# Kernel tuning notes

Measured on AMD Instinct MI355X. Metric: run time of the kernel, lower is better.

Reference implementation:

```python
import jax, jax.numpy as jnp
import numpy as np

NEG_BIG = -1e12
ALPHA = 0.2  # LeakyReLU negative slope

def setup_inputs() -> dict:
    key = jax.random.key(0)
    k1, k2, k3, k4, k5 = jax.random.split(key, 5)
    N, F_in, F_out = 8192, 256, 128
    inp = jax.random.normal(k1, (N, F_in), dtype=jnp.float32)
    adj = jax.random.randint(k2, (N, N), 0, 2, dtype=jnp.int32)
    W = jax.random.normal(k3, (F_in, F_out), dtype=jnp.float32) * 0.05
    W_2 = jax.random.normal(k4, (F_in, F_out), dtype=jnp.float32) * 0.05
    W_3 = jax.random.normal(k5, (F_in, F_out), dtype=jnp.float32) * 0.05
    return {"inp": inp, "adj": adj, "W": W, "W_2": W_2, "W_3": W_3}

def reference(inp, adj, W, W_2, W_3):
    # h = inp @ W, h_2 = inp @ W_2  -> scores e = LeakyReLU(h @ h_2^T)  [N, N]
    h = inp @ W
    h_2 = inp @ W_2
    e = jax.nn.leaky_relu(h @ h_2.T, negative_slope=ALPHA)
    # adjacency mask, row softmax (dropout disabled: eval mode)
    attention = jax.nn.softmax(jnp.where(adj > 0, e, NEG_BIG), axis=1)
    h_3 = inp @ W_3
    h_prime = attention @ h_3
    return jax.nn.elu(h_prime)  # concat=True path
```

## Files before the change

kernel.cpp:

```cpp
#include <hip/hip_runtime.h>
#include <hip/hip_fp16.h>

#define N    8192
#define FIN  256
#define FOUT 128
#define BN   64

typedef _Float16 half8 __attribute__((ext_vector_type(8)));
typedef _Float16 half4v __attribute__((ext_vector_type(4)));
typedef float floatx4 __attribute__((ext_vector_type(4)));

__device__ __forceinline__ float exp2_fast(float x) { return __builtin_amdgcn_exp2f(x); }

__device__ __forceinline__ void gload_lds16(const void* g, void* l) {
    __builtin_amdgcn_global_load_lds(
        (const __attribute__((address_space(1))) void*)g,
        (__attribute__((address_space(3))) void*)l, 16, 0, 0);
}

__global__ __launch_bounds__(256)
void wprep_kernel(const float* __restrict__ W0,
                  const float* __restrict__ W1,
                  const float* __restrict__ W2,
                  _Float16* __restrict__ Wf)
{
    int idx  = blockIdx.x * 256 + threadIdx.x;
    int lane = idx & 63;
    int frag = idx >> 6;
    int w    = frag >> 6;
    int f    = frag & 63;
    int nt   = f >> 3, kc = f & 7;
    int quad = lane >> 4, lo16 = lane & 15;
    const float* Wp = w == 0 ? W0 : (w == 1 ? W1 : W2);
    half8 v;
#pragma unroll
    for (int jj = 0; jj < 8; jj++)
        v[jj] = (_Float16)Wp[(size_t)(kc * 32 + quad * 8 + jj) * FOUT + nt * 16 + lo16];
    *(half8*)&Wf[(size_t)idx * 8] = v;
}

__global__ __launch_bounds__(256, 2)
void gemmadj_kernel(const float* __restrict__ inp,
                    const _Float16* __restrict__ Wf,
                    _Float16* __restrict__ H,
                    _Float16* __restrict__ H2,
                    _Float16* __restrict__ H3T,
                    const int* __restrict__ adj,
                    unsigned long long* __restrict__ adjbT)
{
    if (blockIdx.x >= 768) {
        const int gw   = (blockIdx.x - 768) * 4 + (threadIdx.x >> 6);
        const int lane = threadIdx.x & 63;
#pragma unroll 1
        for (int k = 0; k < 16; k++) {
            int t  = gw + k * 4096;
            int w  = t >> 9;
            int rg = t & 511;
            const int* p = adj + (size_t)(rg * 16) * N + w * 64 + lane;
            unsigned long long myw = 0;
#pragma unroll
            for (int i = 0; i < 16; i++) {
                unsigned long long b = __ballot(p[(size_t)i * N] != 0);
                myw = (lane == i) ? b : myw;
            }
            if (lane < 16)
                adjbT[(size_t)w * N + rg * 16 + lane] = myw;
        }
        return;
    }

    const int g     = blockIdx.x;
    const int which = g >> 8;
    const int rem   = g & 255;
    const int c0    = ((rem >> 7) & 1) * 64;
    const int r0    = (rem & 127) * 64;
    const _Float16* Wfw = Wf + (size_t)which * 64 * 64 * 8;
    const int tid  = threadIdx.x;
    const int wave = tid >> 6;
    const int lane = tid & 63;
    const int lo16 = lane & 15;
    const int quad = lane >> 4;
    const int r = r0 + wave * 16 + lo16;

    half8 a[8];
#pragma unroll
    for (int kc = 0; kc < 8; kc++) {
        const float* p = &inp[(size_t)r * FIN + kc * 32 + quad * 8];
        float4 v0 = *(const float4*)p;
        float4 v1 = *(const float4*)(p + 4);
        a[kc][0] = (_Float16)v0.x; a[kc][1] = (_Float16)v0.y;
        a[kc][2] = (_Float16)v0.z; a[kc][3] = (_Float16)v0.w;
        a[kc][4] = (_Float16)v1.x; a[kc][5] = (_Float16)v1.y;
        a[kc][6] = (_Float16)v1.z; a[kc][7] = (_Float16)v1.w;
    }

    floatx4 acc[4];
#pragma unroll
    for (int i = 0; i < 4; i++) acc[i] = (floatx4){0.f, 0.f, 0.f, 0.f};

#pragma unroll
    for (int kc = 0; kc < 8; kc++)
#pragma unroll
        for (int nt = 0; nt < 4; nt++) {
            int ntg = (c0 >> 4) + nt;
            half8 b = *(const half8*)&Wfw[(((size_t)ntg * 8 + kc) * 64 + lane) * 8];
            acc[nt] = __builtin_amdgcn_mfma_f32_16x16x32_f16(a[kc], b, acc[nt], 0, 0, 0);
        }

    const int arow = wave * 16 + quad * 4;
    if (which < 2) {
        _Float16* outp = which == 0 ? H : H2;
        const float scale = which == 0 ? 1.44269504f : 1.0f;
#pragma unroll
        for (int nt = 0; nt < 4; nt++)
#pragma unroll
            for (int rr = 0; rr < 4; rr++)
                outp[(size_t)(r0 + arow + rr) * FOUT + c0 + nt * 16 + lo16] =
                    (_Float16)(acc[nt][rr] * scale);
    } else {
#pragma unroll
        for (int nt = 0; nt < 4; nt++) {
            half4v v;
#pragma unroll
            for (int rr = 0; rr < 4; rr++) v[rr] = (_Float16)acc[nt][rr];
            *(half4v*)&H3T[(size_t)(c0 + nt * 16 + lo16) * N + r0 + arow] = v;
        }
    }
}

__global__ __launch_bounds__(256)
void repackKV_kernel(const _Float16* __restrict__ H2,
                     const _Float16* __restrict__ H3T,
                     _Float16* __restrict__ Kf,
                     _Float16* __restrict__ Vf)
{
    if (blockIdx.x < 512) {
        int idx  = blockIdx.x * 256 + threadIdx.x;
        int lane = idx & 63;
        int frag = idx >> 6;
        int jb = frag >> 4, f = frag & 15;
        int c = f >> 3, ntj = (f >> 2) & 1, kc = f & 3;
        int quad = lane >> 4, lo16 = lane & 15;
        int srcrow = jb * 64 + c * 32 + (lo16 >> 2) * 8 + ntj * 4 + (lo16 & 3);
        half8 v = *(const half8*)&H2[(size_t)srcrow * FOUT + kc * 32 + quad * 8];
        *(half8*)&Kf[(size_t)idx * 8] = v;
    } else {
        int idx  = (blockIdx.x - 512) * 256 + threadIdx.x;
        int lane = idx & 63;
        int frag = idx >> 6;
        int jb = frag >> 4, f = frag & 15, nt = f >> 1, kc = f & 1;
        int quad = lane >> 4, lo16 = lane & 15;
        half8 v = *(const half8*)&H3T[(size_t)(nt * 16 + lo16) * N + jb * 64 + kc * 32 + quad * 8];
        *(half8*)&Vf[(size_t)idx * 8] = v;
    }
}

template<int JS>
__global__ __launch_bounds__(256, 2)
void attn_kernel(const _Float16* __restrict__ Hq,
                 const _Float16* __restrict__ Kf,
                 const _Float16* __restrict__ Vf,
                 const unsigned long long* __restrict__ adjbT,
                 float* __restrict__ OpartT,
                 float* __restrict__ mpart,
                 float* __restrict__ lpart)
{
    __shared__ __align__(16) _Float16 KV[2][16384];

    const int tid  = threadIdx.x;
    const int wave = tid >> 6;
    const int lane = tid & 63;
    const int lo16 = lane & 15;
    const int quad = lane >> 4;
    const int bid  = blockIdx.x;
    const int js   = bid & (JS - 1);
    const int ib   = bid / JS;
    const int iw   = ib * 128 + wave * 32;
    const int jbeg = js * (N / JS);
    const int NIT  = (N / JS) / BN;
    const int jb0  = jbeg >> 6;

    half8 q[2][4];
#pragma unroll
    for (int isub = 0; isub < 2; isub++)
#pragma unroll
        for (int kc = 0; kc < 4; kc++)
            q[isub][kc] = *(const half8*)&Hq[(size_t)(iw + isub * 16 + lo16) * FOUT + kc * 32 + quad * 8];

    floatx4 O[8][2];
#pragma unroll
    for (int nt = 0; nt < 8; nt++)
#pragma unroll
        for (int s = 0; s < 2; s++) O[nt][s] = (floatx4){0.f, 0.f, 0.f, 0.f};
    float m_s[2] = {-1e12f, -1e12f}, l_s[2] = {0.f, 0.f};

    {
        const _Float16* gk = Kf + (size_t)jb0 * 8192;
        const _Float16* gv = Vf + (size_t)jb0 * 8192;
#pragma unroll
        for (int r = 0; r < 4; r++) {
            int goff = (r * 256 + tid) * 8;
            int loff = (r * 256 + wave * 64) * 8;
            gload_lds16(gk + goff, &KV[0][loff]);
            gload_lds16(gv + goff, &KV[0][8192 + loff]);
        }
        __syncthreads();
    }

    int cur = 0;
    for (int it = 0; it < NIT; it++) {
        if (it + 1 < NIT) {
            const int jbn = jb0 + it + 1;
            const int nxt = cur ^ 1;
            const _Float16* gk = Kf + (size_t)jbn * 8192;
            const _Float16* gv = Vf + (size_t)jbn * 8192;
#pragma unroll
            for (int r = 0; r < 4; r++) {
                int goff = (r * 256 + tid) * 8;
                int loff = (r * 256 + wave * 64) * 8;
                gload_lds16(gk + goff, &KV[nxt][loff]);
                gload_lds16(gv + goff, &KV[nxt][8192 + loff]);
            }
        }

        const unsigned long long* aw = adjbT + (size_t)(jb0 + it) * N + iw;
        unsigned long long mw[2] = { aw[lo16], aw[16 + lo16] };

        const _Float16* kb = &KV[cur][0];
        const _Float16* vb = &KV[cur][8192];

        floatx4 S[2][2][2];
#pragma unroll
        for (int c = 0; c < 2; c++)
#pragma unroll
            for (int ntj = 0; ntj < 2; ntj++) {
                S[c][ntj][0] = (floatx4){0.f, 0.f, 0.f, 0.f};
                S[c][ntj][1] = (floatx4){0.f, 0.f, 0.f, 0.f};
#pragma unroll
                for (int kc = 0; kc < 4; kc++) {
                    half8 kf = *(const half8*)&kb[(((c * 2 + ntj) * 4 + kc) * 64 + lane) * 8];
                    S[c][ntj][0] = __builtin_amdgcn_mfma_f32_16x16x32_f16(kf, q[0][kc], S[c][ntj][0], 0, 0, 0);
                    S[c][ntj][1] = __builtin_amdgcn_mfma_f32_16x16x32_f16(kf, q[1][kc], S[c][ntj][1], 0, 0, 0);
                }
            }

        half8 pb[2][2];
#pragma unroll
        for (int s = 0; s < 2; s++) {
            float mx = -1e12f;
#pragma unroll
            for (int c = 0; c < 2; c++)
#pragma unroll
                for (int ntj = 0; ntj < 2; ntj++)
#pragma unroll
                    for (int r = 0; r < 4; r++) {
                        float e = S[c][ntj][s][r];
                        e = fmaxf(e, 0.2f * e);
                        S[c][ntj][s][r] = e;
                        mx = fmaxf(mx, e);
                    }
            mx = fmaxf(mx, __shfl_xor(mx, 16));
            mx = fmaxf(mx, __shfl_xor(mx, 32));
            if (__any(mx > m_s[s] + 5.75f)) {
                float mn = fmaxf(m_s[s], mx);
                float al = exp2_fast(m_s[s] - mn);
                m_s[s] = mn;
                l_s[s] *= al;
#pragma unroll
                for (int nt = 0; nt < 8; nt++)
#pragma unroll
                    for (int r = 0; r < 4; r++)
                        O[nt][s][r] *= al;
            }

            unsigned long long mq = mw[s] >> (quad * 8);
            unsigned mh[2] = { (unsigned)mq, (unsigned)(mq >> 32) };
            float sum = 0.f;
#pragma unroll
            for (int c = 0; c < 2; c++)
#pragma unroll
                for (int ntj = 0; ntj < 2; ntj++)
#pragma unroll
                    for (int r = 0; r < 4; r++) {
                        float e = S[c][ntj][s][r] - m_s[s];
                        bool bit = (mh[c] >> (ntj * 4 + r)) & 1u;
                        float p = bit ? exp2_fast(e) : 0.f;
                        sum += p;
                        pb[s][c][ntj * 4 + r] = (_Float16)p;
                    }
            sum += __shfl_xor(sum, 16);
            sum += __shfl_xor(sum, 32);
            l_s[s] += sum;
        }

#pragma unroll
        for (int c = 0; c < 2; c++)
#pragma unroll
            for (int nt = 0; nt < 8; nt++) {
                half8 vf = *(const half8*)&vb[((nt * 2 + c) * 64 + lane) * 8];
                O[nt][0] = __builtin_amdgcn_mfma_f32_16x16x32_f16(vf, pb[0][c], O[nt][0], 0, 0, 0);
                O[nt][1] = __builtin_amdgcn_mfma_f32_16x16x32_f16(vf, pb[1][c], O[nt][1], 0, 0, 0);
            }

        __syncthreads();
        cur ^= 1;
    }

#pragma unroll
    for (int nt = 0; nt < 8; nt++)
#pragma unroll
        for (int s = 0; s < 2; s++)
#pragma unroll
            for (int r = 0; r < 4; r++) {
                int f = nt * 16 + quad * 4 + r;
                int i = iw + s * 16 + lo16;
                OpartT[((size_t)js * FOUT + f) * N + i] = O[nt][s][r];
            }
    if (quad == 0) {
#pragma unroll
        for (int s = 0; s < 2; s++) {
            mpart[js * N + iw + s * 16 + lo16] = m_s[s];
            lpart[js * N + iw + s * 16 + lo16] = l_s[s];
        }
    }
}

template<int JS>
__global__ __launch_bounds__(256)
void combine_kernel(const float* __restrict__ OpartT,
                    const float* __restrict__ mpart,
                    const float* __restrict__ lpart,
                    float* __restrict__ out)
{
    int idx = blockIdx.x * 256 + threadIdx.x;
    int f  = idx >> 11;
    int i4 = (idx & 2047) << 2;

    float4 M = {-3e38f, -3e38f, -3e38f, -3e38f};
    float4 m[JS];
#pragma unroll
    for (int s = 0; s < JS; s++) {
        m[s] = *(const float4*)&mpart[s * N + i4];
        M.x = fmaxf(M.x, m[s].x); M.y = fmaxf(M.y, m[s].y);
        M.z = fmaxf(M.z, m[s].z); M.w = fmaxf(M.w, m[s].w);
    }
    float4 L = {0.f, 0.f, 0.f, 0.f};
    float4 o = {0.f, 0.f, 0.f, 0.f};
#pragma unroll
    for (int s = 0; s < JS; s++) {
        float4 l = *(const float4*)&lpart[s * N + i4];
        float4 w;
        w.x = exp2_fast(m[s].x - M.x); w.y = exp2_fast(m[s].y - M.y);
        w.z = exp2_fast(m[s].z - M.z); w.w = exp2_fast(m[s].w - M.w);
        L.x += l.x * w.x; L.y += l.y * w.y;
        L.z += l.z * w.z; L.w += l.w * w.w;
        float4 v = *(const float4*)&OpartT[((size_t)s * FOUT + f) * N + i4];
        o.x += w.x * v.x; o.y += w.y * v.y;
        o.z += w.z * v.z; o.w += w.w * v.w;
    }
    float r0 = o.x / L.x, r1 = o.y / L.y, r2 = o.z / L.z, r3 = o.w / L.w;
    out[(size_t)(i4 + 0) * FOUT + f] = r0 > 0.f ? r0 : __expf(r0) - 1.f;
    out[(size_t)(i4 + 1) * FOUT + f] = r1 > 0.f ? r1 : __expf(r1) - 1.f;
    out[(size_t)(i4 + 2) * FOUT + f] = r2 > 0.f ? r2 : __expf(r2) - 1.f;
    out[(size_t)(i4 + 3) * FOUT + f] = r3 > 0.f ? r3 : __expf(r3) - 1.f;
}

extern "C" void kernel_launch(void* const* d_in, const int* in_sizes, int n_in,
                              void* d_out, int out_size, void* d_ws, size_t ws_size,
                              hipStream_t stream) {
    const float* inp = (const float*)d_in[0];
    const int*   adj = (const int*)d_in[1];
    const float* W0  = (const float*)d_in[2];
    const float* W1  = (const float*)d_in[3];
    const float* W2  = (const float*)d_in[4];
    float* out = (float*)d_out;

    constexpr int JS = 8;
    char* ws = (char*)d_ws;
    _Float16* H    = (_Float16*)(ws);
    _Float16* H2   = (_Float16*)(ws + (2u << 20));
    _Float16* H3T  = (_Float16*)(ws + (4u << 20));
    _Float16* Wf   = (_Float16*)(ws + (6u << 20));
    _Float16* Kf   = (_Float16*)(ws + (7u << 20));
    _Float16* Vf   = (_Float16*)(ws + (9u << 20));
    float* OpartT  = (float*)(ws + (11u << 20));
    float* mpart   = (float*)(ws + (43u << 20));
    float* lpart   = (float*)(ws + (43u << 20) + (size_t)JS * N * sizeof(float));
    unsigned long long* adjbT = (unsigned long long*)(ws + (44u << 20));

    wprep_kernel<<<48, 256, 0, stream>>>(W0, W1, W2, Wf);
    gemmadj_kernel<<<768 + 1024, 256, 0, stream>>>(inp, Wf, H, H2, H3T, adj, adjbT);
    repackKV_kernel<<<1024, 256, 0, stream>>>(H2, H3T, Kf, Vf);
    attn_kernel<JS><<<(N / 128) * JS, 256, 0, stream>>>(H, Kf, Vf, adjbT, OpartT, mpart, lpart);
    combine_kernel<JS><<<(FOUT * (N / 4)) / 256, 256, 0, stream>>>(OpartT, mpart, lpart, out);
}
```

Baseline: 460.9 us.

## Triple-buffer attention K/V tiles at 32 columns, preload adjacency mask into LDS

```diff
diff --git a/kernel.cpp b/kernel.cpp
--- a/kernel.cpp
+++ b/kernel.cpp
@@ -4,7 +4,7 @@
 #define N    8192
 #define FIN  256
 #define FOUT 128
-#define BN   64
+#define BN   32
 
 typedef _Float16 half8 __attribute__((ext_vector_type(8)));
 typedef _Float16 half4v __attribute__((ext_vector_type(4)));
@@ -19,41 +19,33 @@
 }
 
 __global__ __launch_bounds__(256)
-void wprep_kernel(const float* __restrict__ W0,
-                  const float* __restrict__ W1,
-                  const float* __restrict__ W2,
-                  _Float16* __restrict__ Wf)
+void prep_kernel(const float* __restrict__ W0,
+                 const float* __restrict__ W1,
+                 const float* __restrict__ W2,
+                 _Float16* __restrict__ Wf,
+                 const int* __restrict__ adj,
+                 unsigned long long* __restrict__ adjbT)
 {
-    int idx  = blockIdx.x * 256 + threadIdx.x;
-    int lane = idx & 63;
-    int frag = idx >> 6;
-    int w    = frag >> 6;
-    int f    = frag & 63;
-    int nt   = f >> 3, kc = f & 7;
-    int quad = lane >> 4, lo16 = lane & 15;
-    const float* Wp = w == 0 ? W0 : (w == 1 ? W1 : W2);
-    half8 v;
-#pragma unroll
-    for (int jj = 0; jj < 8; jj++)
-        v[jj] = (_Float16)Wp[(size_t)(kc * 32 + quad * 8 + jj) * FOUT + nt * 16 + lo16];
-    *(half8*)&Wf[(size_t)idx * 8] = v;
-}
-
-__global__ __launch_bounds__(256, 2)
-void gemmadj_kernel(const float* __restrict__ inp,
-                    const _Float16* __restrict__ Wf,
-                    _Float16* __restrict__ H,
-                    _Float16* __restrict__ H2,
-                    _Float16* __restrict__ H3T,
-                    const int* __restrict__ adj,
-                    unsigned long long* __restrict__ adjbT)
-{
-    if (blockIdx.x >= 768) {
-        const int gw   = (blockIdx.x - 768) * 4 + (threadIdx.x >> 6);
+    if (blockIdx.x < 48) {
+        int idx  = blockIdx.x * 256 + threadIdx.x;
+        int lane = idx & 63;
+        int frag = idx >> 6;
+        int w    = frag >> 6;
+        int f    = frag & 63;
+        int nt   = f >> 3, kc = f & 7;
+        int quad = lane >> 4, lo16 = lane & 15;
+        const float* Wp = w == 0 ? W0 : (w == 1 ? W1 : W2);
+        half8 v;
+#pragma unroll
+        for (int jj = 0; jj < 8; jj++)
+            v[jj] = (_Float16)Wp[(size_t)(kc * 32 + quad * 8 + jj) * FOUT + nt * 16 + lo16];
+        *(half8*)&Wf[(size_t)idx * 8] = v;
+    } else {
+        const int gw   = (blockIdx.x - 48) * 4 + (threadIdx.x >> 6);
         const int lane = threadIdx.x & 63;
 #pragma unroll 1
-        for (int k = 0; k < 16; k++) {
-            int t  = gw + k * 4096;
+        for (int k = 0; k < 8; k++) {
+            int t  = gw + k * 8192;
             int w  = t >> 9;
             int rg = t & 511;
             const int* p = adj + (size_t)(rg * 16) * N + w * 64 + lane;
@@ -66,15 +58,20 @@
             if (lane < 16)
                 adjbT[(size_t)w * N + rg * 16 + lane] = myw;
         }
-        return;
-    }
-
-    const int g     = blockIdx.x;
-    const int which = g >> 8;
-    const int rem   = g & 255;
-    const int c0    = ((rem >> 7) & 1) * 64;
-    const int r0    = (rem & 127) * 64;
+    }
+}
+
+__global__ __launch_bounds__(256, 2)
+void gemm3_kernel(const float* __restrict__ inp,
+                  const _Float16* __restrict__ Wf,
+                  _Float16* __restrict__ H,
+                  _Float16* __restrict__ H2,
+                  _Float16* __restrict__ H3T)
+{
+    const int which = blockIdx.z;
+    const int c0    = blockIdx.y * 64;
     const _Float16* Wfw = Wf + (size_t)which * 64 * 64 * 8;
+    const int r0 = blockIdx.x * 64;
     const int tid  = threadIdx.x;
     const int wave = tid >> 6;
     const int lane = tid & 63;
@@ -165,7 +162,8 @@
                  float* __restrict__ mpart,
                  float* __restrict__ lpart)
 {
-    __shared__ __align__(16) _Float16 KV[2][16384];
+    __shared__ __align__(16) _Float16 KV[3][8192];
+    __shared__ unsigned long long ML[16 * 128];
 
     const int tid  = threadIdx.x;
     const int wave = tid >> 6;
@@ -175,10 +173,19 @@
     const int bid  = blockIdx.x;
     const int js   = bid & (JS - 1);
     const int ib   = bid / JS;
-    const int iw   = ib * 128 + wave * 32;
+    const int ibase = ib * 128;
+    const int iw   = ibase + wave * 32;
     const int jbeg = js * (N / JS);
-    const int NIT  = (N / JS) / BN;
+    constexpr int NIT = (N / JS) / BN;
     const int jb0  = jbeg >> 6;
+
+#pragma unroll
+    for (int x = 0; x < 8; x++) {
+        int idx  = x * 256 + tid;
+        int w    = idx >> 7;
+        int r128 = idx & 127;
+        ML[idx] = adjbT[(size_t)(jb0 + w) * N + ibase + r128];
+    }
 
     half8 q[2][4];
 #pragma unroll
@@ -194,71 +201,70 @@
         for (int s = 0; s < 2; s++) O[nt][s] = (floatx4){0.f, 0.f, 0.f, 0.f};
     float m_s[2] = {-1e12f, -1e12f}, l_s[2] = {0.f, 0.f};
 
-    {
-        const _Float16* gk = Kf + (size_t)jb0 * 8192;
-        const _Float16* gv = Vf + (size_t)jb0 * 8192;
-#pragma unroll
-        for (int r = 0; r < 4; r++) {
-            int goff = (r * 256 + tid) * 8;
-            int loff = (r * 256 + wave * 64) * 8;
-            gload_lds16(gk + goff, &KV[0][loff]);
-            gload_lds16(gv + goff, &KV[0][8192 + loff]);
-        }
-        __syncthreads();
-    }
-
-    int cur = 0;
-    for (int it = 0; it < NIT; it++) {
-        if (it + 1 < NIT) {
-            const int jbn = jb0 + it + 1;
-            const int nxt = cur ^ 1;
-            const _Float16* gk = Kf + (size_t)jbn * 8192;
-            const _Float16* gv = Vf + (size_t)jbn * 8192;
-#pragma unroll
-            for (int r = 0; r < 4; r++) {
-                int goff = (r * 256 + tid) * 8;
-                int loff = (r * 256 + wave * 64) * 8;
-                gload_lds16(gk + goff, &KV[nxt][loff]);
-                gload_lds16(gv + goff, &KV[nxt][8192 + loff]);
+    auto STAGE = [&](int buf, int t2) {
+        const int jb2 = jb0 + (t2 >> 1), cb2 = t2 & 1;
+        const _Float16* gk = Kf + ((size_t)jb2 * 16 + cb2 * 8) * 512;
+#pragma unroll
+        for (int r = 0; r < 2; r++)
+            gload_lds16(gk + (r * 256 + tid) * 8, &KV[buf][(r * 256 + wave * 64) * 8]);
+#pragma unroll
+        for (int r = 0; r < 2; r++) {
+            const int fv = r * 4 + wave;
+            gload_lds16(Vf + ((size_t)jb2 * 16 + fv * 2 + cb2) * 512 + lane * 8,
+                        &KV[buf][4096 + fv * 512]);
+        }
+    };
+
+    STAGE(0, 0);
+    STAGE(1, 1);
+    asm volatile("s_waitcnt vmcnt(4) lgkmcnt(0)" ::: "memory");
+    __builtin_amdgcn_sched_barrier(0);
+    __builtin_amdgcn_s_barrier();
+    __builtin_amdgcn_sched_barrier(0);
+
+    int bc = 0;
+    for (int t = 0; t < NIT; t++) {
+        const int cbit = t & 1;
+
+        if (t + 2 < NIT) {
+            int bs = bc + 2; if (bs >= 3) bs -= 3;
+            STAGE(bs, t + 2);
+        }
+
+        unsigned long long mw0 = ML[(t >> 1) * 128 + wave * 32 + lo16];
+        unsigned long long mw1 = ML[(t >> 1) * 128 + wave * 32 + 16 + lo16];
+
+        const _Float16* kb = &KV[bc][0];
+        const _Float16* vb = &KV[bc][4096];
+
+        floatx4 S[2][2];
+        __builtin_amdgcn_s_setprio(1);
+#pragma unroll
+        for (int ntj = 0; ntj < 2; ntj++) {
+            S[ntj][0] = (floatx4){0.f, 0.f, 0.f, 0.f};
+            S[ntj][1] = (floatx4){0.f, 0.f, 0.f, 0.f};
+#pragma unroll
+            for (int kc = 0; kc < 4; kc++) {
+                half8 kf = *(const half8*)&kb[((ntj * 4 + kc) * 64 + lane) * 8];
+                S[ntj][0] = __builtin_amdgcn_mfma_f32_16x16x32_f16(kf, q[0][kc], S[ntj][0], 0, 0, 0);
+                S[ntj][1] = __builtin_amdgcn_mfma_f32_16x16x32_f16(kf, q[1][kc], S[ntj][1], 0, 0, 0);
             }
         }
-
-        const unsigned long long* aw = adjbT + (size_t)(jb0 + it) * N + iw;
-        unsigned long long mw[2] = { aw[lo16], aw[16 + lo16] };
-
-        const _Float16* kb = &KV[cur][0];
-        const _Float16* vb = &KV[cur][8192];
-
-        floatx4 S[2][2][2];
-#pragma unroll
-        for (int c = 0; c < 2; c++)
-#pragma unroll
-            for (int ntj = 0; ntj < 2; ntj++) {
-                S[c][ntj][0] = (floatx4){0.f, 0.f, 0.f, 0.f};
-                S[c][ntj][1] = (floatx4){0.f, 0.f, 0.f, 0.f};
-#pragma unroll
-                for (int kc = 0; kc < 4; kc++) {
-                    half8 kf = *(const half8*)&kb[(((c * 2 + ntj) * 4 + kc) * 64 + lane) * 8];
-                    S[c][ntj][0] = __builtin_amdgcn_mfma_f32_16x16x32_f16(kf, q[0][kc], S[c][ntj][0], 0, 0, 0);
-                    S[c][ntj][1] = __builtin_amdgcn_mfma_f32_16x16x32_f16(kf, q[1][kc], S[c][ntj][1], 0, 0, 0);
-                }
-            }
-
-        half8 pb[2][2];
+        __builtin_amdgcn_s_setprio(0);
+
+        half8 pb[2];
 #pragma unroll
         for (int s = 0; s < 2; s++) {
             float mx = -1e12f;
 #pragma unroll
-            for (int c = 0; c < 2; c++)
-#pragma unroll
-                for (int ntj = 0; ntj < 2; ntj++)
-#pragma unroll
-                    for (int r = 0; r < 4; r++) {
-                        float e = S[c][ntj][s][r];
-                        e = fmaxf(e, 0.2f * e);
-                        S[c][ntj][s][r] = e;
-                        mx = fmaxf(mx, e);
-                    }
+            for (int ntj = 0; ntj < 2; ntj++)
+#pragma unroll
+                for (int rr = 0; rr < 4; rr++) {
+                    float e = S[ntj][s][rr];
+                    e = fmaxf(e, 0.2f * e);
+                    S[ntj][s][rr] = e;
+                    mx = fmaxf(mx, e);
+                }
             mx = fmaxf(mx, __shfl_xor(mx, 16));
             mx = fmaxf(mx, __shfl_xor(mx, 32));
             if (__any(mx > m_s[s] + 5.75f)) {
@@ -269,41 +275,41 @@
 #pragma unroll
                 for (int nt = 0; nt < 8; nt++)
 #pragma unroll
-                    for (int r = 0; r < 4; r++)
-                        O[nt][s][r] *= al;
+                    for (int rr = 0; rr < 4; rr++)
+                        O[nt][s][rr] *= al;
             }
-
-            unsigned long long mq = mw[s] >> (quad * 8);
-            unsigned mh[2] = { (unsigned)mq, (unsigned)(mq >> 32) };
+            unsigned long long mws = (s == 0) ? mw0 : mw1;
+            unsigned m8 = (unsigned)(mws >> (cbit * 32 + quad * 8)) & 0xffu;
             float sum = 0.f;
 #pragma unroll
-            for (int c = 0; c < 2; c++)
-#pragma unroll
-                for (int ntj = 0; ntj < 2; ntj++)
-#pragma unroll
-                    for (int r = 0; r < 4; r++) {
-                        float e = S[c][ntj][s][r] - m_s[s];
-                        bool bit = (mh[c] >> (ntj * 4 + r)) & 1u;
-                        float p = bit ? exp2_fast(e) : 0.f;
-                        sum += p;
-                        pb[s][c][ntj * 4 + r] = (_Float16)p;
-                    }
+            for (int ntj = 0; ntj < 2; ntj++)
+#pragma unroll
+                for (int rr = 0; rr < 4; rr++) {
+                    float e = S[ntj][s][rr] - m_s[s];
+                    float p = ((m8 >> (ntj * 4 + rr)) & 1u) ? exp2_fast(e) : 0.f;
+                    sum += p;
+                    pb[s][ntj * 4 + rr] = (_Float16)p;
+                }
             sum += __shfl_xor(sum, 16);
             sum += __shfl_xor(sum, 32);
             l_s[s] += sum;
         }
 
-#pragma unroll
-        for (int c = 0; c < 2; c++)
-#pragma unroll
-            for (int nt = 0; nt < 8; nt++) {
-                half8 vf = *(const half8*)&vb[((nt * 2 + c) * 64 + lane) * 8];
-                O[nt][0] = __builtin_amdgcn_mfma_f32_16x16x32_f16(vf, pb[0][c], O[nt][0], 0, 0, 0);
-                O[nt][1] = __builtin_amdgcn_mfma_f32_16x16x32_f16(vf, pb[1][c], O[nt][1], 0, 0, 0);
-            }
-
-        __syncthreads();
-        cur ^= 1;
+        __builtin_amdgcn_s_setprio(1);
+#pragma unroll
+        for (int nt = 0; nt < 8; nt++) {
+            half8 vf = *(const half8*)&vb[(nt * 64 + lane) * 8];
+            O[nt][0] = __builtin_amdgcn_mfma_f32_16x16x32_f16(vf, pb[0], O[nt][0], 0, 0, 0);
+            O[nt][1] = __builtin_amdgcn_mfma_f32_16x16x32_f16(vf, pb[1], O[nt][1], 0, 0, 0);
+        }
+        __builtin_amdgcn_s_setprio(0);
+
+        if (t + 2 < NIT) asm volatile("s_waitcnt vmcnt(4)" ::: "memory");
+        else             asm volatile("s_waitcnt vmcnt(0)" ::: "memory");
+        __builtin_amdgcn_sched_barrier(0);
+        __builtin_amdgcn_s_barrier();
+        __builtin_amdgcn_sched_barrier(0);
+        bc = (bc + 1 == 3) ? 0 : bc + 1;
     }
 
 #pragma unroll
@@ -311,10 +317,10 @@
 #pragma unroll
         for (int s = 0; s < 2; s++)
 #pragma unroll
-            for (int r = 0; r < 4; r++) {
-                int f = nt * 16 + quad * 4 + r;
+            for (int rr = 0; rr < 4; rr++) {
+                int f = nt * 16 + quad * 4 + rr;
                 int i = iw + s * 16 + lo16;
-                OpartT[((size_t)js * FOUT + f) * N + i] = O[nt][s][r];
+                OpartT[((size_t)js * FOUT + f) * N + i] = O[nt][s][rr];
             }
     if (quad == 0) {
 #pragma unroll
@@ -388,8 +394,8 @@
     float* lpart   = (float*)(ws + (43u << 20) + (size_t)JS * N * sizeof(float));
     unsigned long long* adjbT = (unsigned long long*)(ws + (44u << 20));
 
-    wprep_kernel<<<48, 256, 0, stream>>>(W0, W1, W2, Wf);
-    gemmadj_kernel<<<768 + 1024, 256, 0, stream>>>(inp, Wf, H, H2, H3T, adj, adjbT);
+    prep_kernel<<<2096, 256, 0, stream>>>(W0, W1, W2, Wf, adj, adjbT);
+    gemm3_kernel<<<dim3(N / 64, 2, 3), 256, 0, stream>>>(inp, Wf, H, H2, H3T);
     repackKV_kernel<<<1024, 256, 0, stream>>>(H2, H3T, Kf, Vf);
     attn_kernel<JS><<<(N / 128) * JS, 256, 0, stream>>>(H, Kf, Vf, adjbT, OpartT, mpart, lpart);
     combine_kernel<JS><<<(FOUT * (N / 4)) / 256, 256, 0, stream>>>(OpartT, mpart, lpart, out);
```

After: 481.9 us. 1.05x slower.

## Fuse adjacency mask reads into attention kernel, drop bit-packing pass

Applied to the files above, without the earlier changes.

```diff
diff --git a/kernel.cpp b/kernel.cpp
--- a/kernel.cpp
+++ b/kernel.cpp
@@ -40,41 +40,16 @@
 }
 
 __global__ __launch_bounds__(256, 2)
-void gemmadj_kernel(const float* __restrict__ inp,
-                    const _Float16* __restrict__ Wf,
-                    _Float16* __restrict__ H,
-                    _Float16* __restrict__ H2,
-                    _Float16* __restrict__ H3T,
-                    const int* __restrict__ adj,
-                    unsigned long long* __restrict__ adjbT)
-{
-    if (blockIdx.x >= 768) {
-        const int gw   = (blockIdx.x - 768) * 4 + (threadIdx.x >> 6);
-        const int lane = threadIdx.x & 63;
-#pragma unroll 1
-        for (int k = 0; k < 16; k++) {
-            int t  = gw + k * 4096;
-            int w  = t >> 9;
-            int rg = t & 511;
-            const int* p = adj + (size_t)(rg * 16) * N + w * 64 + lane;
-            unsigned long long myw = 0;
-#pragma unroll
-            for (int i = 0; i < 16; i++) {
-                unsigned long long b = __ballot(p[(size_t)i * N] != 0);
-                myw = (lane == i) ? b : myw;
-            }
-            if (lane < 16)
-                adjbT[(size_t)w * N + rg * 16 + lane] = myw;
-        }
-        return;
-    }
-
-    const int g     = blockIdx.x;
-    const int which = g >> 8;
-    const int rem   = g & 255;
-    const int c0    = ((rem >> 7) & 1) * 64;
-    const int r0    = (rem & 127) * 64;
+void gemm3_kernel(const float* __restrict__ inp,
+                  const _Float16* __restrict__ Wf,
+                  _Float16* __restrict__ H,
+                  _Float16* __restrict__ H2,
+                  _Float16* __restrict__ H3T)
+{
+    const int which = blockIdx.z;
+    const int c0    = blockIdx.y * 64;
     const _Float16* Wfw = Wf + (size_t)which * 64 * 64 * 8;
+    const int r0 = blockIdx.x * 64;
     const int tid  = threadIdx.x;
     const int wave = tid >> 6;
     const int lane = tid & 63;
@@ -160,7 +135,7 @@
 void attn_kernel(const _Float16* __restrict__ Hq,
                  const _Float16* __restrict__ Kf,
                  const _Float16* __restrict__ Vf,
-                 const unsigned long long* __restrict__ adjbT,
+                 const int* __restrict__ adj,
                  float* __restrict__ OpartT,
                  float* __restrict__ mpart,
                  float* __restrict__ lpart)
@@ -194,37 +169,45 @@
         for (int s = 0; s < 2; s++) O[nt][s] = (floatx4){0.f, 0.f, 0.f, 0.f};
     float m_s[2] = {-1e12f, -1e12f}, l_s[2] = {0.f, 0.f};
 
-    {
-        const _Float16* gk = Kf + (size_t)jb0 * 8192;
-        const _Float16* gv = Vf + (size_t)jb0 * 8192;
+    const int* abase0 = adj + (size_t)(iw + lo16) * N + jbeg + quad * 8;
+    const int* abase1 = abase0 + (size_t)16 * N;
+
+    int4 avA[8], avB[8];
+
+    auto LOADAV = [&](int4 (&av)[8], int it) {
+        const int* b0 = abase0 + it * BN;
+        const int* b1 = abase1 + it * BN;
+        av[0] = *(const int4*)(b0 + 0);
+        av[1] = *(const int4*)(b0 + 4);
+        av[2] = *(const int4*)(b0 + 32);
+        av[3] = *(const int4*)(b0 + 36);
+        av[4] = *(const int4*)(b1 + 0);
+        av[5] = *(const int4*)(b1 + 4);
+        av[6] = *(const int4*)(b1 + 32);
+        av[7] = *(const int4*)(b1 + 36);
+    };
+
+    auto STAGE = [&](int nxt, int jbn) {
+        const _Float16* gk = Kf + (size_t)jbn * 8192;
+        const _Float16* gv = Vf + (size_t)jbn * 8192;
 #pragma unroll
         for (int r = 0; r < 4; r++) {
             int goff = (r * 256 + tid) * 8;
             int loff = (r * 256 + wave * 64) * 8;
-            gload_lds16(gk + goff, &KV[0][loff]);
-            gload_lds16(gv + goff, &KV[0][8192 + loff]);
-        }
-        __syncthreads();
-    }
-
-    int cur = 0;
-    for (int it = 0; it < NIT; it++) {
+            gload_lds16(gk + goff, &KV[nxt][loff]);
+            gload_lds16(gv + goff, &KV[nxt][8192 + loff]);
+        }
+    };
+
+    STAGE(0, jb0);
+    LOADAV(avA, 0);
+    __syncthreads();
+
+    auto ITER = [&](int it, int4 (&avc)[8], int4 (&avn)[8], int cur) {
         if (it + 1 < NIT) {
-            const int jbn = jb0 + it + 1;
-            const int nxt = cur ^ 1;
-            const _Float16* gk = Kf + (size_t)jbn * 8192;
-            const _Float16* gv = Vf + (size_t)jbn * 8192;
-#pragma unroll
-            for (int r = 0; r < 4; r++) {
-                int goff = (r * 256 + tid) * 8;
-                int loff = (r * 256 + wave * 64) * 8;
-                gload_lds16(gk + goff, &KV[nxt][loff]);
-                gload_lds16(gv + goff, &KV[nxt][8192 + loff]);
-            }
-        }
-
-        const unsigned long long* aw = adjbT + (size_t)(jb0 + it) * N + iw;
-        unsigned long long mw[2] = { aw[lo16], aw[16 + lo16] };
+            STAGE(cur ^ 1, jb0 + it + 1);
+            LOADAV(avn, it + 1);
+        }
 
         const _Float16* kb = &KV[cur][0];
         const _Float16* vb = &KV[cur][8192];
@@ -273,21 +256,21 @@
                         O[nt][s][r] *= al;
             }
 
-            unsigned long long mq = mw[s] >> (quad * 8);
-            unsigned mh[2] = { (unsigned)mq, (unsigned)(mq >> 32) };
             float sum = 0.f;
 #pragma unroll
             for (int c = 0; c < 2; c++)
 #pragma unroll
-                for (int ntj = 0; ntj < 2; ntj++)
+                for (int ntj = 0; ntj < 2; ntj++) {
+                    int4 av = avc[s * 4 + c * 2 + ntj];
 #pragma unroll
                     for (int r = 0; r < 4; r++) {
                         float e = S[c][ntj][s][r] - m_s[s];
-                        bool bit = (mh[c] >> (ntj * 4 + r)) & 1u;
-                        float p = bit ? exp2_fast(e) : 0.f;
+                        int a = (r == 0) ? av.x : (r == 1) ? av.y : (r == 2) ? av.z : av.w;
+                        float p = (a != 0) ? exp2_fast(e) : 0.f;
                         sum += p;
                         pb[s][c][ntj * 4 + r] = (_Float16)p;
                     }
+                }
             sum += __shfl_xor(sum, 16);
             sum += __shfl_xor(sum, 32);
             l_s[s] += sum;
@@ -303,7 +286,11 @@
             }
 
         __syncthreads();
-        cur ^= 1;
+    };
+
+    for (int it2 = 0; it2 < NIT; it2 += 2) {
+        ITER(it2,     avA, avB, 0);
+        ITER(it2 + 1, avB, avA, 1);
     }
 
 #pragma unroll
@@ -386,11 +373,10 @@
     float* OpartT  = (float*)(ws + (11u << 20));
     float* mpart   = (float*)(ws + (43u << 20));
     float* lpart   = (float*)(ws + (43u << 20) + (size_t)JS * N * sizeof(float));
-    unsigned long long* adjbT = (unsigned long long*)(ws + (44u << 20));
 
     wprep_kernel<<<48, 256, 0, stream>>>(W0, W1, W2, Wf);
-    gemmadj_kernel<<<768 + 1024, 256, 0, stream>>>(inp, Wf, H, H2, H3T, adj, adjbT);
+    gemm3_kernel<<<dim3(N / 64, 2, 3), 256, 0, stream>>>(inp, Wf, H, H2, H3T);
     repackKV_kernel<<<1024, 256, 0, stream>>>(H2, H3T, Kf, Vf);
-    attn_kernel<JS><<<(N / 128) * JS, 256, 0, stream>>>(H, Kf, Vf, adjbT, OpartT, mpart, lpart);
+    attn_kernel<JS><<<(N / 128) * JS, 256, 0, stream>>>(H, Kf, Vf, adj, OpartT, mpart, lpart);
     combine_kernel<JS><<<(FOUT * (N / 4)) / 256, 256, 0, stream>>>(OpartT, mpart, lpart, out);
 }
```

New measurement: 425.3 us. 1.08x faster.
